# Performance work log

Measured on AMD Instinct MI355X. Metric: run time of the kernel, lower is better.

## Reference

```python
import jax, jax.numpy as jnp
import numpy as np

INF = 1e8
EPS = 1e-6
STRIDES = (8, 16, 32, 64, 128)
FEAT_SIZES = ((100, 128), (50, 64), (25, 32), (13, 16), (7, 8))
NUM_CLASSES = 81  # args.num_classes + 1
BG = NUM_CLASSES
TOPK1, TOPK2 = 3, 1
RATIO = 0.9
FRACTION = 0.5
B, G = 16, 32
NPER = [h * w for h, w in FEAT_SIZES]
OFFS = np.cumsum([0] + NPER)


def gen_trf():
    j = [2 ** i for i in range(8)]
    r1 = 1 + 6 * j[0]; r2 = r1 + 2 * j[1]
    p2 = r2 + 2 * j[2] * 3; r3 = p2 + 2 * j[2]
    p3 = r3 + 2 * j[3] * 3; r4 = p3 + 2 * j[3]
    p4 = r4 + 2 * j[4] * 5; r5 = p4 + 2 * j[4]
    p5 = r5 + 2 * j[5] * 2
    p6 = p5 + 2 * j[6]; p7 = p6 + 2 * j[7]
    return [p2, p3, p4, p5, p6, p7]


def make_points_rfields():
    trfs = gen_trf()
    pts, rfs = [], []
    for lvl, (h, w) in enumerate(FEAT_SIZES):
        s = STRIDES[lvl]
        xs = jnp.arange(w, dtype=jnp.float32) * s + s // 2
        ys = jnp.arange(h, dtype=jnp.float32) * s + s // 2
        Y, X = jnp.meshgrid(ys, xs, indexing='ij')
        p = jnp.stack([X.reshape(-1), Y.reshape(-1)], -1)
        pts.append(p)
        rf = trfs[lvl + 1] * FRACTION  # fpn_layer == 'p3' -> rfnum = lvl + 1
        rfs.append(jnp.concatenate([p - rf / 2, p + rf / 2], -1))
    return jnp.concatenate(pts, 0), jnp.concatenate(rfs, 0)


def kl_overlaps(gts, anc):
    # BboxDistanceMetric mode='kl': Gaussian KL divergence -> 1/(1+kl); (G, N)
    c1 = (gts[:, :2] + gts[:, 2:]) / 2
    c2 = (anc[:, :2] + anc[:, 2:]) / 2
    w1 = gts[:, 2] - gts[:, 0] + EPS; h1 = gts[:, 3] - gts[:, 1] + EPS
    w2 = anc[:, 2] - anc[:, 0] + EPS; h2 = anc[:, 3] - anc[:, 1] + EPS
    dx = c1[:, None, 0] - c2[None, :, 0]; dy = c1[:, None, 1] - c2[None, :, 1]
    w1s = (w1 ** 2)[:, None]; h1s = (h1 ** 2)[:, None]
    w2s = (w2 ** 2)[None, :]; h2s = (h2 ** 2)[None, :]
    kl = (w2s / w1s + h2s / h1s + 4 * dx ** 2 / w1s + 4 * dy ** 2 / h1s
          + jnp.log(w1s / w2s) + jnp.log(h1s / h2s) - 2) / 2
    return 1.0 / (1.0 + kl)


def hie_assign(rf1, rf2, gts):
    ov1 = kl_overlaps(gts, rf1)
    ov2 = kl_overlaps(gts, rf2)
    N = rf1.shape[0]; Gn = gts.shape[0]
    max_ov = ov1.max(0)
    assigned = jnp.where((max_ov >= 0) & (max_ov < 0.8), 0, -1).astype(jnp.int32)
    gt_ids = jnp.arange(1, Gn + 1, dtype=jnp.int32)
    _, i1 = jax.lax.top_k(ov1, TOPK1)  # (G, k1)
    s1 = jnp.full((N,), -1, jnp.int32).at[i1.reshape(-1)].max(jnp.repeat(gt_ids, TOPK1))
    assigned = jnp.where(s1 > 0, s1, assigned)
    _, i2 = jax.lax.top_k(ov2, TOPK2)  # (G, k2) second hierarchy overrides
    s2 = jnp.full((N,), -1, jnp.int32).at[i2.reshape(-1)].max(jnp.repeat(gt_ids, TOPK2))
    return jnp.where(s2 > 0, s2, assigned)


def target_single(gts, glabels, points, rf1, rf2):
    Gn = gts.shape[0]
    assigned = hie_assign(rf1, rf2, gts)  # (N,) 1-based gt index, 0/-1 = bg
    areas = (gts[:, 2] - gts[:, 0]) * (gts[:, 3] - gts[:, 1])
    mask = (assigned - 1)[:, None] == jnp.arange(Gn)[None, :]
    am = jnp.where(mask, areas[None, :], INF)
    min_area = am.min(1); mi = jnp.argmin(am, 1)
    lab = jnp.where(min_area >= INF, BG, glabels[mi])
    g = gts[mi]
    bt = jnp.stack([points[:, 0] - g[:, 0], points[:, 1] - g[:, 1],
                    g[:, 2] - points[:, 0], g[:, 3] - points[:, 1]], -1)
    return lab, bt


def diou_loss(pred, tgt):
    lt = jnp.maximum(pred[:, :2], tgt[:, :2])
    rb = jnp.minimum(pred[:, 2:], tgt[:, 2:])
    wh = jnp.clip(rb - lt, 0.0)
    ov = wh[:, 0] * wh[:, 1]
    ap = (pred[:, 2] - pred[:, 0]) * (pred[:, 3] - pred[:, 1])
    ag = (tgt[:, 2] - tgt[:, 0]) * (tgt[:, 3] - tgt[:, 1])
    ious = ov / (ap + ag - ov + EPS)
    elt = jnp.minimum(pred[:, :2], tgt[:, :2])
    erb = jnp.maximum(pred[:, 2:], tgt[:, 2:])
    ewh = jnp.clip(erb - elt, 0.0)
    c2 = ewh[:, 0] ** 2 + ewh[:, 1] ** 2 + EPS
    rho2 = ((pred[:, 0] + pred[:, 2] - tgt[:, 0] - tgt[:, 2]) ** 2
            + (pred[:, 1] + pred[:, 3] - tgt[:, 1] - tgt[:, 3]) ** 2) / 4
    return 1.0 - (ious - rho2 / c2)


def _forward(cls_l, bbox_l, ctr_l, gt_bboxes, gt_labels):
    points, rf1 = make_points_rfields()
    c = (rf1[:, :2] + rf1[:, 2:]) / 2
    wh = (rf1[:, 2:] - rf1[:, :2]) * RATIO
    rf2 = jnp.concatenate([c - wh / 2, c + wh / 2], -1)
    labels_all, targets_all = jax.vmap(target_single, (0, 0, None, None, None))(
        gt_bboxes, gt_labels, points, rf1, rf2)
    labels_all = jax.lax.stop_gradient(labels_all)
    targets_all = jax.lax.stop_gradient(targets_all)
    # flatten level-major, image-minor (matches torch.cat order in loss)
    fc = jnp.concatenate([t.transpose(0, 2, 3, 1).reshape(-1, NUM_CLASSES) for t in cls_l], 0)
    fb = jnp.concatenate([t.transpose(0, 2, 3, 1).reshape(-1, 4) for t in bbox_l], 0)
    fo = jnp.concatenate([t.transpose(0, 2, 3, 1).reshape(-1) for t in ctr_l], 0)
    fl = jnp.concatenate([labels_all[:, OFFS[i]:OFFS[i + 1]].reshape(-1) for i in range(5)], 0)
    ft = jnp.concatenate([targets_all[:, OFFS[i]:OFFS[i + 1]].reshape(-1, 4) for i in range(5)], 0)
    fp = jnp.concatenate([jnp.tile(points[OFFS[i]:OFFS[i + 1]], (B, 1)) for i in range(5)], 0)
    pos = fl < BG
    posf = pos.astype(fc.dtype)
    num_pos = jnp.maximum(posf.sum(), 1.0)
    # sigmoid focal loss (alpha=0.25, gamma=2); bg label -> all-zero one-hot
    tgt = jax.nn.one_hot(fl, NUM_CLASSES, dtype=fc.dtype)
    p = jax.nn.sigmoid(fc)
    pt = (1 - p) * tgt + p * (1 - tgt)
    fw = (0.25 * tgt + 0.75 * (1 - tgt)) * pt ** 2
    bce = jnp.maximum(fc, 0) - fc * tgt + jnp.log1p(jnp.exp(-jnp.abs(fc)))
    loss_cls = (bce * fw).sum() / num_pos
    # centerness target (sanitized on negatives to avoid nan)
    bt = jnp.where(pos[:, None], ft, 1.0)
    lr_min = jnp.minimum(bt[:, 0], bt[:, 2]); lr_max = jnp.maximum(bt[:, 0], bt[:, 2])
    tb_min = jnp.minimum(bt[:, 1], bt[:, 3]); tb_max = jnp.maximum(bt[:, 1], bt[:, 3])
    ctr_tgt = jnp.sqrt(jnp.clip((lr_min / lr_max) * (tb_min / tb_max), 0.0)) * posf
    denom = jnp.maximum(ctr_tgt.sum(), 1e-6)
    # decode distances to boxes and DIoU loss weighted by centerness
    x, y = fp[:, 0], fp[:, 1]
    pb = jnp.stack([x - fb[:, 0], y - fb[:, 1], x + fb[:, 2], y + fb[:, 3]], -1)
    tb_box = jnp.stack([x - bt[:, 0], y - bt[:, 1], x + bt[:, 2], y + bt[:, 3]], -1)
    loss_bbox = (diou_loss(pb, tb_box) * ctr_tgt).sum() / denom
    # centerness BCE-with-logits, averaged by num_pos
    bce_c = jnp.maximum(fo, 0) - fo * ctr_tgt + jnp.log1p(jnp.exp(-jnp.abs(fo)))
    loss_ctr = (bce_c * posf).sum() / num_pos
    return jnp.stack([loss_cls, loss_bbox, loss_ctr])


def setup_inputs() -> dict:
    key = jax.random.key(0)
    ks = jax.random.split(key, 24)
    cls_l = [jax.random.normal(ks[i], (B, NUM_CLASSES, h, w), jnp.float32) - 4.0
             for i, (h, w) in enumerate(FEAT_SIZES)]
    bbox_l = [jax.random.uniform(ks[5 + i], (B, 4, h, w), jnp.float32) * 64.0 + 1.0
              for i, (h, w) in enumerate(FEAT_SIZES)]
    ctr_l = [jax.random.normal(ks[10 + i], (B, 1, h, w), jnp.float32)
             for i, (h, w) in enumerate(FEAT_SIZES)]
    cx = jax.random.uniform(ks[15], (B, G)) * 1000.0 + 12.0
    cy = jax.random.uniform(ks[16], (B, G)) * 776.0 + 12.0
    w = jax.random.uniform(ks[17], (B, G)) * 240.0 + 8.0
    h = jax.random.uniform(ks[18], (B, G)) * 240.0 + 8.0
    gt_bboxes = jnp.stack([cx - w / 2, cy - h / 2, cx + w / 2, cy + h / 2], -1)
    gt_labels = jax.random.randint(ks[19], (B, G), 0, 80)
    d = {}
    for i in range(5):
        d[f'cls{i}'] = cls_l[i]; d[f'bbox{i}'] = bbox_l[i]; d[f'ctr{i}'] = ctr_l[i]
    d['gt_bboxes'] = gt_bboxes
    d['gt_labels'] = gt_labels
    return d


def reference(cls0, cls1, cls2, cls3, cls4, bbox0, bbox1, bbox2, bbox3, bbox4,
              ctr0, ctr1, ctr2, ctr3, ctr4, gt_bboxes, gt_labels):
    return _forward([cls0, cls1, cls2, cls3, cls4],
                    [bbox0, bbox1, bbox2, bbox3, bbox4],
                    [ctr0, ctr1, ctr2, ctr3, ctr4], gt_bboxes, gt_labels)
```

## Files before the change

### kernel.cpp

```cpp
#include <hip/hip_runtime.h>
#include <math.h>
#include <limits.h>

#pragma clang fp contract(off)

#define N_ANCH 17064
#define BATCH  16
#define NGT    32
#define EPSF   1e-6f

#define NPB     512
#define NSTREAM 1536
#define SSTRIDE (NSTREAM * 256)
#define SUBN    96
#define L2E 1.44269504088896340736f
#define LN2 0.69314718055994530942f

#define C1   4147200
#define C2   5184000
#define C3   5443200
#define C4   5510592
#define TOT4 5528736

#define CTR_IMG 0
#define CTR_SUB 16
#define CTR_GLB 32

__device__ __forceinline__ float fexp2(float x){ return __builtin_amdgcn_exp2f(x); }
__device__ __forceinline__ float flog2(float x){ return __builtin_amdgcn_logf(x); }
__device__ __forceinline__ float frcp (float x){ return __builtin_amdgcn_rcpf(x); }

__device__ __forceinline__ void astore_u32(unsigned int* p, unsigned int v) {
  __hip_atomic_store(p, v, __ATOMIC_RELAXED, __HIP_MEMORY_SCOPE_AGENT);
}
__device__ __forceinline__ unsigned int aload_u32(const unsigned int* p) {
  return __hip_atomic_load(p, __ATOMIC_RELAXED, __HIP_MEMORY_SCOPE_AGENT);
}
__device__ __forceinline__ void astore_u64(unsigned long long* p, unsigned long long v) {
  __hip_atomic_store(p, v, __ATOMIC_RELAXED, __HIP_MEMORY_SCOPE_AGENT);
}
__device__ __forceinline__ unsigned long long aload_u64(const unsigned long long* p) {
  return __hip_atomic_load(p, __ATOMIC_RELAXED, __HIP_MEMORY_SCOPE_AGENT);
}
#define VMCNT0() asm volatile("s_waitcnt vmcnt(0)" ::: "memory")

struct Geo { int lvl; int j; int HW; float px; float py; };

__device__ __forceinline__ Geo geom(int n) {
  Geo g;
  if (n < 12800)      { g.lvl=0; g.j=n;       g.HW=12800; g.px=(float)((g.j & 127)*8 + 4);   g.py=(float)((g.j >> 7)*8 + 4);   }
  else if (n < 16000) { g.lvl=1; g.j=n-12800; g.HW=3200;  g.px=(float)((g.j & 63)*16 + 8);   g.py=(float)((g.j >> 6)*16 + 8);  }
  else if (n < 16800) { g.lvl=2; g.j=n-16000; g.HW=800;   g.px=(float)((g.j & 31)*32 + 16);  g.py=(float)((g.j >> 5)*32 + 16); }
  else if (n < 17008) { g.lvl=3; g.j=n-16800; g.HW=208;   g.px=(float)((g.j & 15)*64 + 32);  g.py=(float)((g.j >> 4)*64 + 32); }
  else                { g.lvl=4; g.j=n-17008; g.HW=56;    g.px=(float)((g.j & 7)*128 + 64);  g.py=(float)((g.j >> 3)*128 + 64);}
  return g;
}

__device__ __forceinline__ bool bet(float av, int ai, float bv, int bi) {
  return (av < bv) || (av == bv && ai < bi);
}

__device__ __forceinline__ void insert3min(float* v, int* i, float nv, int ni) {
  if (nv < v[0])      { v[2]=v[1]; i[2]=i[1]; v[1]=v[0]; i[1]=i[0]; v[0]=nv; i[0]=ni; }
  else if (nv < v[1]) { v[2]=v[1]; i[2]=i[1]; v[1]=nv; i[1]=ni; }
  else                { v[2]=nv; i[2]=ni; }
}

__device__ __forceinline__ void insert3tie(float* v, int* i, float nv, int ni) {
  if (!bet(nv, ni, v[2], i[2])) return;
  if (bet(nv, ni, v[0], i[0]))      { v[2]=v[1]; i[2]=i[1]; v[1]=v[0]; i[1]=i[0]; v[0]=nv; i[0]=ni; }
  else if (bet(nv, ni, v[1], i[1])) { v[2]=v[1]; i[2]=i[1]; v[1]=nv; i[1]=ni; }
  else                              { v[2]=nv; i[2]=ni; }
}

__device__ __forceinline__ float negterm(float x) {
  float ax = fabsf(x);
  float e  = fexp2(ax * -L2E);
  float r  = frcp(1.0f + e);
  float p  = (x >= 0.0f) ? r : e * r;
  float sp = fmaxf(x, 0.0f) + flog2(1.0f + e) * LN2;
  return 0.75f * (p * p) * sp;
}

__device__ __forceinline__ float negterm4(float4 f) {
  return ((negterm(f.x) + negterm(f.y)) + (negterm(f.z) + negterm(f.w)));
}

__device__ __forceinline__ const float4* lvl_addr(int i, const float4* s0, const float4* s1,
                                                  const float4* s2, const float4* s3,
                                                  const float4* s4) {
  if (i < C1)      return s0 + i;
  else if (i < C2) return s1 + (i - C1);
  else if (i < C3) return s2 + (i - C2);
  else if (i < C4) return s3 + (i - C3);
  else             return s4 + (i - C4);
}

__global__ void zeroK(int* __restrict__ ctr) {
  int i = threadIdx.x;
  if (i < 33) ctr[i] = 0;
}

__device__ __forceinline__ void final_combine(const unsigned long long* __restrict__ bpart,
                                              const unsigned long long* __restrict__ gsum,
                                              float* __restrict__ out,
                                              double* R, int t) {
  if (t < 16) {
    R[t]      = __longlong_as_double(aload_u64(&gsum[t]));
    R[16+t]   = __longlong_as_double(aload_u64(&bpart[t*5+0]));
    R[32+t]   = __longlong_as_double(aload_u64(&bpart[t*5+1]));
    R[48+t]   = __longlong_as_double(aload_u64(&bpart[t*5+2]));
    R[64+t]   = __longlong_as_double(aload_u64(&bpart[t*5+3]));
    R[80+t]   = __longlong_as_double(aload_u64(&bpart[t*5+4]));
  }
  __syncthreads();
  if (t == 0) {
    double sc = 0.0, sp = 0.0, sct = 0.0, sdi = 0.0, scb = 0.0;
    for (int i = 0; i < 16; ++i) sc += R[i];
    for (int i = 0; i < 16; ++i) {
      sc  += R[16+i];
      sp  += R[32+i];
      sct += R[48+i];
      sdi += R[64+i];
      scb += R[80+i];
    }
    double np_ = sp > 1.0 ? sp : 1.0;
    double dn  = sct > 1e-6 ? sct : 1e-6;
    out[0] = (float)(sc / np_);
    out[1] = (float)(sdi / dn);
    out[2] = (float)(scb / np_);
  }
}

__global__ __launch_bounds__(256) void fusedK(
    const float4* __restrict__ gtb, const int* __restrict__ glab,
    const float* __restrict__ c0, const float* __restrict__ c1, const float* __restrict__ c2,
    const float* __restrict__ c3, const float* __restrict__ c4,
    const float* __restrict__ bb0, const float* __restrict__ bb1, const float* __restrict__ bb2,
    const float* __restrict__ bb3, const float* __restrict__ bb4,
    const float* __restrict__ ct0, const float* __restrict__ ct1, const float* __restrict__ ct2,
    const float* __restrict__ ct3, const float* __restrict__ ct4,
    unsigned int* __restrict__ win, unsigned int* __restrict__ part,
    unsigned long long* __restrict__ bpart, unsigned long long* __restrict__ gsum,
    int* __restrict__ ctr, float* __restrict__ out) {
  __shared__ char smem[9216];
  __shared__ int sflag, sflag2;

  int t  = threadIdx.x;
  int bi = blockIdx.x;

  if (bi >= NPB) {
    int sb = bi - NPB;
    const float4* s0 = (const float4*)c0;
    const float4* s1 = (const float4*)c1;
    const float4* s2 = (const float4*)c2;
    const float4* s3 = (const float4*)c3;
    const float4* s4 = (const float4*)c4;
    int i = sb * 256 + t;
    float acc0 = 0.0f, acc1 = 0.0f;

    float4 a0 = s0[i];
    float4 a1 = s0[i +     SSTRIDE];
    float4 a2 = s0[i + 2 * SSTRIDE];
    float4 a3 = s0[i + 3 * SSTRIDE];
    float4 a4 = s0[i + 4 * SSTRIDE];

    float4 b0 = s0[i + 5 * SSTRIDE];
    float4 b1 = s0[i + 6 * SSTRIDE];
    float4 b2 = s0[i + 7 * SSTRIDE];
    float4 b3 = s0[i + 8 * SSTRIDE];
    float4 b4 = s0[i + 9 * SSTRIDE];

    acc0 += negterm4(a0);
    acc1 += negterm4(a1);
    acc0 += negterm4(a2);
    acc1 += negterm4(a3);
    acc0 += negterm4(a4);

    int  j0 = i + 10 * SSTRIDE, j1 = i + 11 * SSTRIDE, j2 = i + 12 * SSTRIDE;
    int  j3 = i + 13 * SSTRIDE, j4 = i + 14 * SSTRIDE;
    bool m4 = j4 < TOT4;
    float4 e0 = *lvl_addr(j0, s0, s1, s2, s3, s4);
    float4 e1 = *lvl_addr(j1, s0, s1, s2, s3, s4);
    float4 e2 = *lvl_addr(j2, s0, s1, s2, s3, s4);
    float4 e3 = *lvl_addr(j3, s0, s1, s2, s3, s4);
    float4 e4 = *lvl_addr(m4 ? j4 : 0, s0, s1, s2, s3, s4);

    acc0 += negterm4(b0);
    acc1 += negterm4(b1);
    acc0 += negterm4(b2);
    acc1 += negterm4(b3);
    acc0 += negterm4(b4);

    acc0 += negterm4(e0);
    acc1 += negterm4(e1);
    acc0 += negterm4(e2);
    acc1 += negterm4(e3);
    acc0 += m4 ? negterm4(e4) : 0.0f;

    float* sh = (float*)smem;
    sh[t] = acc0 + acc1;
    __syncthreads();
    #pragma unroll
    for (int off = 128; off > 0; off >>= 1) {
      if (t < off) sh[t] += sh[t + off];
      __syncthreads();
    }
    if (t == 0) {
      astore_u32(&part[sb], __float_as_uint(sh[0]));
      VMCNT0();
      int old = atomicAdd(&ctr[CTR_SUB + (sb & 15)], 1);
      sflag = (old == SUBN - 1);
    }
    __syncthreads();
    if (!sflag) return;

    int g = sb & 15;
    double* rr = (double*)(smem + 1024);
    if (t < 128) {
      double v = 0.0;
      if (t < SUBN) v = (double)__uint_as_float(aload_u32(&part[g + (t << 4)]));
      rr[t] = v;
    }
    __syncthreads();
    #pragma unroll
    for (int off = 64; off > 0; off >>= 1) {
      if (t < off) rr[t] += rr[t + off];
      __syncthreads();
    }
    if (t == 0) {
      astore_u64(&gsum[g], (unsigned long long)__double_as_longlong(rr[0]));
      VMCNT0();
      int old2 = atomicAdd(&ctr[CTR_GLB], 1);
      sflag2 = (old2 == 31);
    }
    __syncthreads();
    if (sflag2) final_combine(bpart, gsum, out, (double*)smem, t);
    return;
  }

  int blk = bi;
  int b = blk >> 5, g = blk & 31;
  {
    float* sv = (float*)smem;
    int*   si = (int*)(smem + 3072);
    float* tv = (float*)(smem + 6144);
    int*   ti = (int*)(smem + 7168);

    float4 GB = gtb[b * NGT + g];
    float c1x = (GB.x + GB.z) * 0.5f, c1y = (GB.y + GB.w) * 0.5f;
    float w1 = GB.z - GB.x + EPSF, h1 = GB.w - GB.y + EPSF;
    float w1s = w1 * w1, h1s = h1 * h1;
    float iw = 1.0f / w1s, ih = 1.0f / h1s;
    float iws = iw + ih;
    float Lg = logf(w1s) + logf(h1s);
    float Ay = 4.0f * ih;
    float Axc = 4.0f * iw;

    float v1[3] = {INFINITY, INFINITY, INFINITY};
    int   i1[3] = {INT_MAX, INT_MAX, INT_MAX};
    float v2 = INFINITY; int i2 = INT_MAX;

    #define DO_LEVEL(BASE, LGW, H, STRIDE, RF) do {                             \
      const int W_ = 1 << (LGW);                                                \
      float w2a = (RF) + 1e-6f;          float w2sa = w2a * w2a;                \
      float w2b = (RF) * 0.9f + 1e-6f;   float w2sb = w2b * w2b;                \
      float K1 = w2sa * iws + Lg - 2.0f * logf(w2sa) - 2.0f;                    \
      float K2 = w2sb * iws + Lg - 2.0f * logf(w2sb) - 2.0f;                    \
      int col = t & (W_ - 1);                                                   \
      float px = (float)(col * (STRIDE) + (STRIDE) / 2);                        \
      float dx = c1x - px;                                                      \
      float kx1 = Axc * dx * dx + K1;                                           \
      float kx2 = Axc * dx * dx + K2;                                           \
      int rstep = 256 >> (LGW);                                                 \
      for (int row = t >> (LGW); row < (H); row += rstep) {                     \
        float py = (float)(row * (STRIDE) + (STRIDE) / 2);                      \
        float dy = c1y - py;                                                    \
        float dy2 = dy * dy;                                                    \
        float k1 = fmaf(Ay, dy2, kx1);                                          \
        float k2 = fmaf(Ay, dy2, kx2);                                          \
        int n = (BASE) + (row << (LGW)) + col;                                  \
        if (k1 < v1[2]) insert3min(v1, i1, k1, n);                              \
        if (k2 < v2) { v2 = k2; i2 = n; }                                       \
      }                                                                         \
    } while (0)

    DO_LEVEL(0,     7, 100,   8,  45.5f);
    DO_LEVEL(12800, 6,  50,  16, 133.5f);
    DO_LEVEL(16000, 5,  25,  32, 213.5f);
    DO_LEVEL(16800, 4,  13,  64, 277.5f);
    DO_LEVEL(17008, 3,   7, 128, 405.5f);
    #undef DO_LEVEL

    sv[t*3+0] = v1[0]; sv[t*3+1] = v1[1]; sv[t*3+2] = v1[2];
    si[t*3+0] = i1[0]; si[t*3+1] = i1[1]; si[t*3+2] = i1[2];
    tv[t] = v2; ti[t] = i2;
    __syncthreads();
    for (int off = 128; off > 0; off >>= 1) {
      if (t < off) {
        #pragma unroll
        for (int k = 0; k < 3; ++k)
          insert3tie(&sv[t * 3], &si[t * 3], sv[(t + off) * 3 + k], si[(t + off) * 3 + k]);
        if (bet(tv[t + off], ti[t + off], tv[t], ti[t])) { tv[t] = tv[t + off]; ti[t] = ti[t + off]; }
      }
      __syncthreads();
    }
    if (t == 0) {
      astore_u32(&win[blk * 4 + 0], (unsigned int)si[0]);
      astore_u32(&win[blk * 4 + 1], (unsigned int)si[1]);
      astore_u32(&win[blk * 4 + 2], (unsigned int)si[2]);
      astore_u32(&win[blk * 4 + 3], (unsigned int)ti[0]);
      VMCNT0();
      int old = atomicAdd(&ctr[CTR_IMG + b], 1);
      sflag = (old == 31);
    }
    __syncthreads();
  }
  if (!sflag) return;

  unsigned int* ukeys = (unsigned int*)smem;
  double* r0 = (double*)(smem + 512);
  double* r1 = (double*)(smem + 1536);
  double* r2 = (double*)(smem + 2560);
  double* r3 = (double*)(smem + 3584);
  double* r4 = (double*)(smem + 4608);

  if (t < 128) {
    int gg = t >> 2, s = t & 3;
    unsigned int n = aload_u32(&win[b * 128 + gg * 4 + s]);
    unsigned int pri = ((s == 3) ? 32u : 0u) + (unsigned int)gg;
    ukeys[t] = (n << 6) | pri;
  }
  __syncthreads();

  double a_cls = 0.0, a_pos = 0.0, a_ctr = 0.0, a_diou = 0.0, a_cbce = 0.0;

  if (t < 128) {
    unsigned int me = ukeys[t];
    unsigned int nn = me >> 6;
    bool alive = true;
    #pragma unroll 8
    for (int j = 0; j < 128; ++j) {
      unsigned int o = ukeys[j];
      if ((o >> 6) == nn && o > me) alive = false;
    }
    if (alive) {
      int n = (int)nn;
      int gg = (int)(me & 31u);
      int lab = glab[b * NGT + gg];
      float4 gb = gtb[b * NGT + gg];
      Geo G = geom(n);

      const float* bb; const float* ct; const float* cp;
      if (G.lvl == 0)      { bb = bb0; ct = ct0; cp = c0; }
      else if (G.lvl == 1) { bb = bb1; ct = ct1; cp = c1; }
      else if (G.lvl == 2) { bb = bb2; ct = ct2; cp = c2; }
      else if (G.lvl == 3) { bb = bb3; ct = ct3; cp = c3; }
      else                 { bb = bb4; ct = ct4; cp = c4; }

      const float* bp = bb + b * 4 * G.HW + G.j;
      float f0 = bp[0];
      float f1 = bp[G.HW];
      float f2 = bp[2 * G.HW];
      float f3 = bp[3 * G.HW];
      float fo = ct[b * G.HW + G.j];
      float xc = cp[((size_t)(b * 81 + lab)) * G.HW + G.j];

      {
        float ax = fabsf(xc);
        float e  = fexp2(ax * -L2E);
        float r  = frcp(1.0f + e);
        float p  = (xc >= 0.0f) ? r : e * r;
        float sp = fmaxf(xc, 0.0f) + flog2(1.0f + e) * LN2;
        float neg = 0.75f * (p * p) * sp;
        float omp = 1.0f - p;
        float pos = 0.25f * (omp * omp) * (sp - xc);
        a_cls += (double)(pos - neg);
      }

      float tx = G.px - gb.x, ty = G.py - gb.y, tz = gb.z - G.px, tw = gb.w - G.py;

      float lr_min = fminf(tx, tz), lr_max = fmaxf(tx, tz);
      float tb_min = fminf(ty, tw), tb_max = fmaxf(ty, tw);
      float prod = (lr_min / lr_max) * (tb_min / tb_max);
      float ctrt = sqrtf(fmaxf(prod, 0.0f));

      float pb0 = G.px - f0, pb1 = G.py - f1, pb2 = G.px + f2, pb3 = G.py + f3;
      float tb0 = G.px - tx, tb1 = G.py - ty, tb2 = G.px + tz, tb3 = G.py + tw;

      float ltx = fmaxf(pb0, tb0), lty = fmaxf(pb1, tb1);
      float rbx = fminf(pb2, tb2), rby = fminf(pb3, tb3);
      float whx = fmaxf(rbx - ltx, 0.0f), why = fmaxf(rby - lty, 0.0f);
      float ovl = whx * why;
      float ap = (pb2 - pb0) * (pb3 - pb1);
      float ag = (tb2 - tb0) * (tb3 - tb1);
      float ious = ovl / (ap + ag - ovl + EPSF);
      float eltx = fminf(pb0, tb0), elty = fminf(pb1, tb1);
      float erbx = fmaxf(pb2, tb2), erby = fmaxf(pb3, tb3);
      float ewx = fmaxf(erbx - eltx, 0.0f), ewy = fmaxf(erby - elty, 0.0f);
      float c2v = ewx * ewx + ewy * ewy + EPSF;
      float sx = pb0 + pb2 - tb0 - tb2;
      float sy = pb1 + pb3 - tb1 - tb3;
      float rho2 = (sx * sx + sy * sy) * 0.25f;
      float dl = 1.0f - (ious - rho2 / c2v);

      a_pos  += 1.0;
      a_ctr  += (double)ctrt;
      a_diou += (double)(dl * ctrt);
      a_cbce += (double)(fmaxf(fo, 0.0f) - fo * ctrt + log1pf(expf(-fabsf(fo))));
    }
  }

  if (t < 128) { r0[t] = a_cls; r1[t] = a_pos; r2[t] = a_ctr; r3[t] = a_diou; r4[t] = a_cbce; }
  __syncthreads();
  #pragma unroll
  for (int off = 64; off > 0; off >>= 1) {
    if (t < off) {
      r0[t] += r0[t + off]; r1[t] += r1[t + off]; r2[t] += r2[t + off];
      r3[t] += r3[t + off]; r4[t] += r4[t + off];
    }
    __syncthreads();
  }

  if (t == 0) {
    astore_u64(&bpart[b * 5 + 0], (unsigned long long)__double_as_longlong(r0[0]));
    astore_u64(&bpart[b * 5 + 1], (unsigned long long)__double_as_longlong(r1[0]));
    astore_u64(&bpart[b * 5 + 2], (unsigned long long)__double_as_longlong(r2[0]));
    astore_u64(&bpart[b * 5 + 3], (unsigned long long)__double_as_longlong(r3[0]));
    astore_u64(&bpart[b * 5 + 4], (unsigned long long)__double_as_longlong(r4[0]));
    VMCNT0();
    int old2 = atomicAdd(&ctr[CTR_GLB], 1);
    sflag2 = (old2 == 31);
  }
  __syncthreads();
  if (sflag2) final_combine(bpart, gsum, out, (double*)smem, t);
}

extern "C" void kernel_launch(void* const* d_in, const int* in_sizes, int n_in,
                              void* d_out, int out_size, void* d_ws, size_t ws_size,
                              hipStream_t stream) {
  (void)in_sizes; (void)n_in; (void)out_size; (void)ws_size;
  const float* cls[5] = {(const float*)d_in[0],  (const float*)d_in[3],  (const float*)d_in[6],
                         (const float*)d_in[9],  (const float*)d_in[12]};
  const float* bbx[5] = {(const float*)d_in[1],  (const float*)d_in[4],  (const float*)d_in[7],
                         (const float*)d_in[10], (const float*)d_in[13]};
  const float* ctr_[5] = {(const float*)d_in[2],  (const float*)d_in[5],  (const float*)d_in[8],
                          (const float*)d_in[11], (const float*)d_in[14]};
  const float4* gtb = (const float4*)d_in[15];
  const int* glab = (const int*)d_in[16];

  char* ws = (char*)d_ws;
  unsigned int*       win   = (unsigned int*)ws;
  unsigned int*       part  = (unsigned int*)(ws + 8192);
  unsigned long long* bpart = (unsigned long long*)(ws + 16384);
  unsigned long long* gsum  = (unsigned long long*)(ws + 17024);
  int*                cnts  = (int*)(ws + 17152);

  zeroK<<<1, 64, 0, stream>>>(cnts);
  fusedK<<<NPB + NSTREAM, 256, 0, stream>>>(
      gtb, glab,
      cls[0], cls[1], cls[2], cls[3], cls[4],
      bbx[0], bbx[1], bbx[2], bbx[3], bbx[4],
      ctr_[0], ctr_[1], ctr_[2], ctr_[3], ctr_[4],
      win, part, bpart, gsum, cnts, (float*)d_out);
}
```

Before: 42.88 us.

## Stream negative-class loads through LDS with direct global-to-LDS pipelined loads

```diff
diff --git a/kernel.cpp b/kernel.cpp
--- a/kernel.cpp
+++ b/kernel.cpp
@@ -43,6 +43,7 @@
   return __hip_atomic_load(p, __ATOMIC_RELAXED, __HIP_MEMORY_SCOPE_AGENT);
 }
 #define VMCNT0() asm volatile("s_waitcnt vmcnt(0)" ::: "memory")
+#define WAITVM(N) asm volatile("s_waitcnt vmcnt(" #N ")" ::: "memory")
 
 struct Geo { int lvl; int j; int HW; float px; float py; };
 
@@ -132,7 +133,7 @@
   }
 }
 
-__global__ __launch_bounds__(256) void fusedK(
+__global__ __launch_bounds__(256, 8) void fusedK(
     const float4* __restrict__ gtb, const int* __restrict__ glab,
     const float* __restrict__ c0, const float* __restrict__ c1, const float* __restrict__ c2,
     const float* __restrict__ c3, const float* __restrict__ c4,
@@ -143,7 +144,8 @@
     unsigned int* __restrict__ win, unsigned int* __restrict__ part,
     unsigned long long* __restrict__ bpart, unsigned long long* __restrict__ gsum,
     int* __restrict__ ctr, float* __restrict__ out) {
-  __shared__ char smem[9216];
+  __shared__ float4 smem4[1088];
+  char* smem = (char*)smem4;
   __shared__ int sflag, sflag2;
 
   int t  = threadIdx.x;
@@ -151,54 +153,57 @@
 
   if (bi >= NPB) {
     int sb = bi - NPB;
+    int l = t & 63, w = t >> 6;
+    int base = sb * 256 + t;
     const float4* s0 = (const float4*)c0;
     const float4* s1 = (const float4*)c1;
     const float4* s2 = (const float4*)c2;
     const float4* s3 = (const float4*)c3;
     const float4* s4 = (const float4*)c4;
-    int i = sb * 256 + t;
+    float4 (*sbuf)[4][64] = (float4 (*)[4][64])smem4;
     float acc0 = 0.0f, acc1 = 0.0f;
 
-    float4 a0 = s0[i];
-    float4 a1 = s0[i +     SSTRIDE];
-    float4 a2 = s0[i + 2 * SSTRIDE];
-    float4 a3 = s0[i + 3 * SSTRIDE];
-    float4 a4 = s0[i + 4 * SSTRIDE];
-
-    float4 b0 = s0[i + 5 * SSTRIDE];
-    float4 b1 = s0[i + 6 * SSTRIDE];
-    float4 b2 = s0[i + 7 * SSTRIDE];
-    float4 b3 = s0[i + 8 * SSTRIDE];
-    float4 b4 = s0[i + 9 * SSTRIDE];
-
-    acc0 += negterm4(a0);
-    acc1 += negterm4(a1);
-    acc0 += negterm4(a2);
-    acc1 += negterm4(a3);
-    acc0 += negterm4(a4);
-
-    int  j0 = i + 10 * SSTRIDE, j1 = i + 11 * SSTRIDE, j2 = i + 12 * SSTRIDE;
-    int  j3 = i + 13 * SSTRIDE, j4 = i + 14 * SSTRIDE;
-    bool m4 = j4 < TOT4;
-    float4 e0 = *lvl_addr(j0, s0, s1, s2, s3, s4);
-    float4 e1 = *lvl_addr(j1, s0, s1, s2, s3, s4);
-    float4 e2 = *lvl_addr(j2, s0, s1, s2, s3, s4);
-    float4 e3 = *lvl_addr(j3, s0, s1, s2, s3, s4);
-    float4 e4 = *lvl_addr(m4 ? j4 : 0, s0, s1, s2, s3, s4);
-
-    acc0 += negterm4(b0);
-    acc1 += negterm4(b1);
-    acc0 += negterm4(b2);
-    acc1 += negterm4(b3);
-    acc0 += negterm4(b4);
-
-    acc0 += negterm4(e0);
-    acc1 += negterm4(e1);
-    acc0 += negterm4(e2);
-    acc1 += negterm4(e3);
-    acc0 += m4 ? negterm4(e4) : 0.0f;
-
-    float* sh = (float*)smem;
+    #define ISSUE(K, SLOT) do {                                                   \
+      const float4* g_;                                                           \
+      if ((K) <= 9)       g_ = s0 + (base + (K) * SSTRIDE);                       \
+      else if ((K) <= 13) g_ = lvl_addr(base + (K) * SSTRIDE, s0, s1, s2, s3, s4);\
+      else { int ii_ = base + 14 * SSTRIDE;                                       \
+             g_ = lvl_addr(ii_ < TOT4 ? ii_ : TOT4 - 1, s0, s1, s2, s3, s4); }    \
+      __builtin_amdgcn_global_load_lds(                                           \
+          (const __attribute__((address_space(1))) unsigned int*)g_,              \
+          (__attribute__((address_space(3))) unsigned int*)&sbuf[SLOT][w][0],     \
+          16, 0, 0);                                                              \
+    } while (0)
+
+    #define CONSUME(K, SLOT) do {                                                 \
+      float4 v_ = sbuf[SLOT][w][l];                                               \
+      if ((K) == 14) {                                                            \
+        int ii_ = base + 14 * SSTRIDE;                                            \
+        if (ii_ < TOT4) acc0 += negterm4(v_);                                     \
+      } else if (((K) & 1) == 0) acc0 += negterm4(v_);                            \
+      else                       acc1 += negterm4(v_);                            \
+    } while (0)
+
+    ISSUE(0, 0); ISSUE(1, 1); ISSUE(2, 2);
+    ISSUE(3, 3);  WAITVM(3); CONSUME(0, 0);
+    ISSUE(4, 0);  WAITVM(3); CONSUME(1, 1);
+    ISSUE(5, 1);  WAITVM(3); CONSUME(2, 2);
+    ISSUE(6, 2);  WAITVM(3); CONSUME(3, 3);
+    ISSUE(7, 3);  WAITVM(3); CONSUME(4, 0);
+    ISSUE(8, 0);  WAITVM(3); CONSUME(5, 1);
+    ISSUE(9, 1);  WAITVM(3); CONSUME(6, 2);
+    ISSUE(10, 2); WAITVM(3); CONSUME(7, 3);
+    ISSUE(11, 3); WAITVM(3); CONSUME(8, 0);
+    ISSUE(12, 0); WAITVM(3); CONSUME(9, 1);
+    ISSUE(13, 1); WAITVM(3); CONSUME(10, 2);
+    ISSUE(14, 2); WAITVM(3); CONSUME(11, 3);
+    WAITVM(2); CONSUME(12, 0);
+    WAITVM(1); CONSUME(13, 1);
+    WAITVM(0); CONSUME(14, 2);
+    #undef ISSUE
+    #undef CONSUME
+
+    float* sh = (float*)(smem + 16384);
     sh[t] = acc0 + acc1;
     __syncthreads();
     #pragma unroll
@@ -216,7 +221,7 @@
     if (!sflag) return;
 
     int g = sb & 15;
-    double* rr = (double*)(smem + 1024);
+    double* rr = (double*)(smem + 16384);
     if (t < 128) {
       double v = 0.0;
       if (t < SUBN) v = (double)__uint_as_float(aload_u32(&part[g + (t << 4)]));
@@ -235,7 +240,7 @@
       sflag2 = (old2 == 31);
     }
     __syncthreads();
-    if (sflag2) final_combine(bpart, gsum, out, (double*)smem, t);
+    if (sflag2) final_combine(bpart, gsum, out, (double*)(smem + 16384), t);
     return;
   }
 
```

Measured after the change: 45.94 us. 1.07x slower.
